# Kernel tuning notes

Hardware: AMD Instinct MI355X
Metric: run time of the kernel (lower is better)

## Reference

```python
import jax, jax.numpy as jnp
import numpy as np

TOKENS = 32768
HIDDEN = 2048
N_EXPERTS = 128
TOP_K = 8
NORM_TOPK_PROB = True


def setup_inputs() -> dict:
    key = jax.random.key(0)
    k1, k2 = jax.random.split(key)
    hidden_states = jax.random.normal(k1, (TOKENS, HIDDEN), dtype=jnp.float32)
    # router weight [num_experts, hidden_dim]; small init like a trained gate
    weight = jax.random.normal(k2, (N_EXPERTS, HIDDEN), dtype=jnp.float32) * 0.02
    return {"hidden_states": hidden_states, "weight": weight}


def reference(hidden_states, weight):
    # flatten tokens (already [T, H])
    x = hidden_states.reshape(-1, HIDDEN)
    # router logits: [T, E]
    logits = jnp.einsum("th,eh->te", x, weight)
    # softmax in float32 (matches dtype=torch.float)
    probs = jax.nn.softmax(logits.astype(jnp.float32), axis=-1)
    # top-k over experts
    top_val, top_idx = jax.lax.top_k(probs, TOP_K)  # [T, K], [T, K]
    if NORM_TOPK_PROB:
        top_val = top_val / jnp.sum(top_val, axis=-1, keepdims=True)
    top_val = top_val.astype(probs.dtype)
    # scatter renormalized weights into dense [T, E] score tensor
    rows = jnp.arange(x.shape[0])[:, None]  # [T, 1]
    scores = jnp.zeros_like(probs).at[rows, top_idx].set(top_val)
    return scores, top_idx
```

## Files before the change

### kernel.cpp

```cpp
#include <hip/hip_runtime.h>
#include <hip/hip_bf16.h>

#define NT   32768
#define NH   2048
#define NE   128
#define TOPK 8
#define BT   64
#define BK   32
#define NKT  (NH / BK)
#define BND    6.0e-4f
#define TWO_B  (2.0f * BND)

#define WS_W_OFF   64
#define WS_REC_U32 262160

typedef __attribute__((ext_vector_type(8))) short bf16x8;
typedef __attribute__((ext_vector_type(4))) float f32x4;

static __device__ __forceinline__ unsigned short f2bf(float f) {
    __hip_bfloat16 h = __float2bfloat16(f);
    return *reinterpret_cast<unsigned short*>(&h);
}

typedef __attribute__((address_space(3))) unsigned int lds_uint;
typedef const __attribute__((address_space(1))) unsigned int glb_uint;
static __device__ __forceinline__ void gld16(const void* g, void* l) {
    __builtin_amdgcn_global_load_lds((glb_uint*)g, (lds_uint*)l, 16, 0, 0);
}

__global__ __launch_bounds__(256) void prep_w_kernel(
    const float* __restrict__ W, unsigned short* __restrict__ Wt)
{
    int g = blockIdx.x * 256 + threadIdx.x;
    int t = g >> 10;
    int m = g & 1023;
    int i = m >> 6;
    int l = m & 63;
    int r = 8 * i + (l >> 3);
    int u = (l & 7) ^ (l >> 3);
    int s = u >> 2;
    int koff = (u & 3) * 8;
    const float* src = W + (size_t)r * NH + t * BK + koff;
    float4 f0 = *(const float4*)src;
    float4 f1 = *(const float4*)(src + 4);
    float f[8] = {f0.x, f0.y, f0.z, f0.w, f1.x, f1.y, f1.z, f1.w};
    bf16x8 o;
    #pragma unroll
    for (int e = 0; e < 8; ++e) {
        unsigned short h = f2bf(f[e]);
        if (s == 0) o[e] = (short)h;
        else {
            float fh = __builtin_bit_cast(float, ((unsigned int)h) << 16);
            o[e] = (short)f2bf(f[e] - fh);
        }
    }
    *(bf16x8*)(Wt + (size_t)g * 8) = o;
}

__global__ __launch_bounds__(256, 2) void router_gemm_kernel(
    const float* __restrict__ X, const unsigned short* __restrict__ Wt,
    float* __restrict__ out, unsigned int* __restrict__ ws)
{
    __shared__ __align__(16) char smem[49152];

    const int tid  = threadIdx.x;
    const int t0   = blockIdx.x * BT;
    const int lane = tid & 63;
    const int wid  = tid >> 6;
    const int wr   = wid >> 1, wc = wid & 1;
    const int l15  = lane & 15, lhi = lane >> 4;
    const int l8   = lane >> 3, l7 = lane & 7;
    const int xu   = l7 ^ l8;

    const char* Xg = (const char*)X;
    const char* Wg = (const char*)Wt;

    f32x4 acc[2][4];
    #pragma unroll
    for (int i = 0; i < 2; ++i)
        #pragma unroll
        for (int j = 0; j < 4; ++j) acc[i][j] = (f32x4){0.f, 0.f, 0.f, 0.f};

    #define STAGE(KT, B) do {                                                   \
        char* Xb_ = smem + (B) * 24576;                                         \
        char* Wb_ = Xb_ + 8192;                                                 \
        _Pragma("unroll")                                                       \
        for (int q = 0; q < 2; ++q) {                                           \
            int i_ = wid * 2 + q;                                               \
            const char* s_ = Xg + (size_t)(t0 + 8 * i_ + l8) * 8192             \
                             + (size_t)(KT) * 128 + xu * 16;                    \
            gld16(s_, Xb_ + i_ * 1024);                                         \
        }                                                                       \
        _Pragma("unroll")                                                       \
        for (int q = 0; q < 4; ++q) {                                           \
            int i_ = wid * 4 + q;                                               \
            const char* s_ = Wg + (size_t)(KT) * 16384 + i_ * 1024 + lane * 16; \
            gld16(s_, Wb_ + i_ * 1024);                                         \
        }                                                                       \
    } while (0)

    STAGE(0, 0);
    __syncthreads();

    for (int kt = 0; kt < NKT; ++kt) {
        const int cur = kt & 1;
        if (kt + 1 < NKT) STAGE(kt + 1, cur ^ 1);

        const char* Xb = smem + cur * 24576;
        const char* Wb = Xb + 8192;

        bf16x8 ah[2], al[2];
        #pragma unroll
        for (int i = 0; i < 2; ++i) {
            int ar = wr * 32 + i * 16 + l15;
            int r7 = ar & 7;
            const char* rp = Xb + ar * 128;
            float4 fa = *(const float4*)(rp + (((2 * lhi) ^ r7) * 16));
            float4 fb = *(const float4*)(rp + (((2 * lhi + 1) ^ r7) * 16));
            float f[8] = {fa.x, fa.y, fa.z, fa.w, fb.x, fb.y, fb.z, fb.w};
            #pragma unroll
            for (int e = 0; e < 8; ++e) {
                unsigned short h = f2bf(f[e]);
                ah[i][e] = (short)h;
                float fh = __builtin_bit_cast(float, ((unsigned int)h) << 16);
                al[i][e] = (short)f2bf(f[e] - fh);
            }
        }
        bf16x8 bw[4][2];
        #pragma unroll
        for (int j = 0; j < 4; ++j) {
            int br = wc * 64 + j * 16 + l15;
            int r7 = br & 7;
            const char* rp = Wb + br * 128;
            bw[j][0] = *(const bf16x8*)(rp + ((lhi ^ r7) * 16));
            bw[j][1] = *(const bf16x8*)(rp + (((4 + lhi) ^ r7) * 16));
        }
        #pragma unroll
        for (int i = 0; i < 2; ++i)
            #pragma unroll
            for (int j = 0; j < 4; ++j) {
                acc[i][j] = __builtin_amdgcn_mfma_f32_16x16x32_bf16(ah[i], bw[j][0], acc[i][j], 0, 0, 0);
                acc[i][j] = __builtin_amdgcn_mfma_f32_16x16x32_bf16(al[i], bw[j][0], acc[i][j], 0, 0, 0);
                acc[i][j] = __builtin_amdgcn_mfma_f32_16x16x32_bf16(ah[i], bw[j][1], acc[i][j], 0, 0, 0);
            }
        __syncthreads();
    }

    float* lg = (float*)smem;
    #pragma unroll
    for (int i = 0; i < 2; ++i)
        #pragma unroll
        for (int j = 0; j < 4; ++j)
            #pragma unroll
            for (int q = 0; q < 4; ++q) {
                int tr = wr * 32 + i * 16 + lhi * 4 + q;
                int ec = wc * 64 + j * 16 + l15;
                lg[tr * 129 + ec] = acc[i][j][q];
            }

    float* scoreBase = out + (size_t)t0 * NE;
    #pragma unroll
    for (int q = 0; q < 8; ++q) {
        int i = tid + q * 256;
        *(float4*)(scoreBase + (size_t)i * 4) = make_float4(0.f, 0.f, 0.f, 0.f);
    }
    __syncthreads();

    if (tid < BT) {
        const float* row = lg + tid * 129;
        float tv[13]; int ti[13];
        #pragma unroll
        for (int k = 0; k < 13; ++k) { tv[k] = -3.0e38f; ti[k] = 0; }
        for (int e = 0; e < NE; ++e) {
            float v = row[e];
            if (v > tv[12]) {
                float cv = v; int ci = e;
                #pragma unroll
                for (int s = 0; s < 13; ++s) {
                    if (cv > tv[s]) {
                        float t1 = tv[s]; int t2 = ti[s];
                        tv[s] = cv; ti[s] = ci; cv = t1; ci = t2;
                    }
                }
            }
        }
        bool flag = false;
        #pragma unroll
        for (int k = 0; k < 8; ++k) flag |= (tv[k] - tv[k + 1] < TWO_B);

        float pv[8]; float ksum = 0.f;
        #pragma unroll
        for (int k = 0; k < 8; ++k) { pv[k] = expf(tv[k] - tv[0]); ksum += pv[k]; }
        const int tg = t0 + tid;
        float* srow = out + (size_t)tg * NE;
        float* irow = out + (size_t)NT * NE + (size_t)tg * TOPK;
        #pragma unroll
        for (int k = 0; k < 8; ++k) {
            srow[ti[k]] = pv[k] / ksum;
            irow[k] = (float)ti[k];
        }

        if (flag) {
            unsigned int cnt;
            unsigned int idw[4] = {0u, 0u, 0u, 0u};
            float thr = tv[7] - TWO_B;
            if (tv[12] >= thr) {
                cnt = 0xFFu;
            } else {
                cnt = 0;
                #pragma unroll
                for (int k = 0; k < 13; ++k) {
                    if (k < 8 || tv[k] >= thr) {
                        idw[cnt >> 2] |= ((unsigned int)ti[k]) << ((cnt & 3) * 8);
                        ++cnt;
                    }
                }
            }
            unsigned int slot = atomicAdd(ws, 1u);
            unsigned int* rec = ws + WS_REC_U32 + slot * 8;
            rec[0] = (unsigned int)tg;
            rec[1] = cnt;
            rec[2] = idw[0]; rec[3] = idw[1]; rec[4] = idw[2]; rec[5] = idw[3];
        }
    }
}

__global__ __launch_bounds__(256) void finalize_kernel(
    const float* __restrict__ X, const float* __restrict__ W,
    float* __restrict__ out, const unsigned int* __restrict__ ws)
{
    __shared__ float  xs[2048];
    __shared__ double cv[128];
    __shared__ int    cid[128];
    __shared__ float  ovals[8];
    __shared__ int    oidx[8];

    const int tid = threadIdx.x;
    const int lane = tid & 63, w = tid >> 6;
    const unsigned int n = ws[0];

    for (unsigned int rI = blockIdx.x; rI < n; rI += gridDim.x) {
        const unsigned int* rec = ws + WS_REC_U32 + rI * 8;
        const int tg = (int)rec[0];
        const unsigned int cnt = rec[1];
        const unsigned char* ids = (const unsigned char*)(rec + 2);
        const int nc = (cnt == 0xFFu) ? NE : (int)cnt;

        #pragma unroll
        for (int q = 0; q < 2; ++q) {
            int i = tid + q * 256;
            *(float4*)(xs + i * 4) = *(const float4*)(X + (size_t)tg * NH + i * 4);
        }
        __syncthreads();

        for (int c = w; c < nc; c += 4) {
            int e = (cnt == 0xFFu) ? c : (int)ids[c];
            const float* wrow = W + (size_t)e * NH;
            double s = 0.0;
            #pragma unroll
            for (int m = 0; m < 8; ++m) {
                float4 wv = *(const float4*)(wrow + m * 256 + lane * 4);
                float4 xv = *(const float4*)(xs + m * 256 + lane * 4);
                s = fma((double)xv.x, (double)wv.x, s);
                s = fma((double)xv.y, (double)wv.y, s);
                s = fma((double)xv.z, (double)wv.z, s);
                s = fma((double)xv.w, (double)wv.w, s);
            }
            #pragma unroll
            for (int off = 32; off >= 1; off >>= 1) s += __shfl_xor(s, off);
            if (lane == 0) { cv[c] = s; cid[c] = e; }
        }
        __syncthreads();

        if (tid == 0) {
            double lv[8];
            #pragma unroll
            for (int k = 0; k < 8; ++k) {
                double best = -1.0e300; int bi = 1 << 30, bc = 0;
                for (int c = 0; c < nc; ++c) {
                    double v = cv[c]; int e = cid[c];
                    if (v > best || (v == best && e < bi)) { best = v; bi = e; bc = c; }
                }
                lv[k] = best; oidx[k] = bi; cv[bc] = -1.0e301;
            }
            double m = lv[0], sum = 0.0, p[8];
            #pragma unroll
            for (int k = 0; k < 8; ++k) { p[k] = exp(lv[k] - m); sum += p[k]; }
            #pragma unroll
            for (int k = 0; k < 8; ++k) ovals[k] = (float)(p[k] / sum);
        }
        __syncthreads();

        float* srow = out + (size_t)tg * NE;
        if (tid < NE) {
            float val = 0.f;
            #pragma unroll
            for (int k = 0; k < 8; ++k) if (oidx[k] == tid) val = ovals[k];
            srow[tid] = val;
        }
        if (tid < TOPK) out[(size_t)NT * NE + (size_t)tg * TOPK + tid] = (float)oidx[tid];
        __syncthreads();
    }
}

extern "C" void kernel_launch(void* const* d_in, const int* in_sizes, int n_in,
                              void* d_out, int out_size, void* d_ws, size_t ws_size,
                              hipStream_t stream) {
    const float* X = (const float*)d_in[0];
    const float* W = (const float*)d_in[1];
    float* out = (float*)d_out;
    unsigned char* wsb = (unsigned char*)d_ws;
    unsigned short* Wt = (unsigned short*)(wsb + WS_W_OFF);

    hipMemsetAsync(d_ws, 0, 64, stream);
    prep_w_kernel<<<256, 256, 0, stream>>>(W, Wt);
    router_gemm_kernel<<<NT / BT, 256, 0, stream>>>(X, Wt, out, (unsigned int*)d_ws);
    finalize_kernel<<<1024, 256, 0, stream>>>(X, W, out, (const unsigned int*)d_ws);
}
```

Measured before the change: 232.2 us.

## Use 512-thread blocks with triple-buffered LDS pipeline and fine-grained vmcnt waits

The router GEMM block grows from 256 to 512 threads, so each of the 8 waves computes a 16x64 tile instead of 32x64. The LDS double buffer becomes a rotating triple buffer that prefetches two k-tiles ahead. The full __syncthreads is replaced with s_waitcnt vmcnt(3) plus a raw barrier, so loads for the newest stage can stay in flight. The aim is more latency hiding and more waves, at the cost of more LDS per block (72KB), less register reuse per wave, and a pipeline whose correctness depends on the exact vmcnt counts.

```diff
diff --git a/kernel.cpp b/kernel.cpp
--- a/kernel.cpp
+++ b/kernel.cpp
@@ -8,6 +8,7 @@
 #define BT   64
 #define BK   32
 #define NKT  (NH / BK)
+#define BUFB 24576
 #define BND    6.0e-4f
 #define TWO_B  (2.0f * BND)
 
@@ -57,11 +58,11 @@
     *(bf16x8*)(Wt + (size_t)g * 8) = o;
 }
 
-__global__ __launch_bounds__(256, 2) void router_gemm_kernel(
+__global__ __launch_bounds__(512, 4) void router_gemm_kernel(
     const float* __restrict__ X, const unsigned short* __restrict__ Wt,
     float* __restrict__ out, unsigned int* __restrict__ ws)
 {
-    __shared__ __align__(16) char smem[49152];
+    __shared__ __align__(16) char smem[73728];
 
     const int tid  = threadIdx.x;
     const int t0   = blockIdx.x * BT;
@@ -75,44 +76,39 @@
     const char* Xg = (const char*)X;
     const char* Wg = (const char*)Wt;
 
-    f32x4 acc[2][4];
+    f32x4 acc[4];
     #pragma unroll
-    for (int i = 0; i < 2; ++i)
-        #pragma unroll
-        for (int j = 0; j < 4; ++j) acc[i][j] = (f32x4){0.f, 0.f, 0.f, 0.f};
-
-    #define STAGE(KT, B) do {                                                   \
-        char* Xb_ = smem + (B) * 24576;                                         \
-        char* Wb_ = Xb_ + 8192;                                                 \
-        _Pragma("unroll")                                                       \
-        for (int q = 0; q < 2; ++q) {                                           \
-            int i_ = wid * 2 + q;                                               \
-            const char* s_ = Xg + (size_t)(t0 + 8 * i_ + l8) * 8192             \
-                             + (size_t)(KT) * 128 + xu * 16;                    \
-            gld16(s_, Xb_ + i_ * 1024);                                         \
-        }                                                                       \
-        _Pragma("unroll")                                                       \
-        for (int q = 0; q < 4; ++q) {                                           \
-            int i_ = wid * 4 + q;                                               \
-            const char* s_ = Wg + (size_t)(KT) * 16384 + i_ * 1024 + lane * 16; \
-            gld16(s_, Wb_ + i_ * 1024);                                         \
-        }                                                                       \
-    } while (0)
-
-    STAGE(0, 0);
-    __syncthreads();
-
+    for (int j = 0; j < 4; ++j) acc[j] = (f32x4){0.f, 0.f, 0.f, 0.f};
+
+    auto stage = [&](int kt, char* base) {
+        char* Xb_ = base;
+        char* Wb_ = base + 8192;
+        const char* sx_ = Xg + (size_t)(t0 + 8 * wid + l8) * 8192
+                          + (size_t)kt * 128 + xu * 16;
+        gld16(sx_, Xb_ + wid * 1024);
+        #pragma unroll
+        for (int q = 0; q < 2; ++q) {
+            int i_ = wid * 2 + q;
+            gld16(Wg + (size_t)kt * 16384 + i_ * 1024 + lane * 16, Wb_ + i_ * 1024);
+        }
+    };
+
+    stage(0, smem);
+    stage(1, smem + BUFB);
+    asm volatile("s_waitcnt vmcnt(3)" ::: "memory");
+    __builtin_amdgcn_s_barrier();
+
+    int rd = 0, st = 2 * BUFB;
     for (int kt = 0; kt < NKT; ++kt) {
-        const int cur = kt & 1;
-        if (kt + 1 < NKT) STAGE(kt + 1, cur ^ 1);
-
-        const char* Xb = smem + cur * 24576;
+        const bool do_stage = (kt + 2 < NKT);
+        if (do_stage) stage(kt + 2, smem + st);
+
+        const char* Xb = smem + rd;
         const char* Wb = Xb + 8192;
 
-        bf16x8 ah[2], al[2];
-        #pragma unroll
-        for (int i = 0; i < 2; ++i) {
-            int ar = wr * 32 + i * 16 + l15;
+        bf16x8 ah, al;
+        {
+            int ar = wr * 16 + l15;
             int r7 = ar & 7;
             const char* rp = Xb + ar * 128;
             float4 fa = *(const float4*)(rp + (((2 * lhi) ^ r7) * 16));
@@ -121,9 +117,9 @@
             #pragma unroll
             for (int e = 0; e < 8; ++e) {
                 unsigned short h = f2bf(f[e]);
-                ah[i][e] = (short)h;
+                ah[e] = (short)h;
                 float fh = __builtin_bit_cast(float, ((unsigned int)h) << 16);
-                al[i][e] = (short)f2bf(f[e] - fh);
+                al[e] = (short)f2bf(f[e] - fh);
             }
         }
         bf16x8 bw[4][2];
@@ -136,32 +132,34 @@
             bw[j][1] = *(const bf16x8*)(rp + (((4 + lhi) ^ r7) * 16));
         }
         #pragma unroll
-        for (int i = 0; i < 2; ++i)
-            #pragma unroll
-            for (int j = 0; j < 4; ++j) {
-                acc[i][j] = __builtin_amdgcn_mfma_f32_16x16x32_bf16(ah[i], bw[j][0], acc[i][j], 0, 0, 0);
-                acc[i][j] = __builtin_amdgcn_mfma_f32_16x16x32_bf16(al[i], bw[j][0], acc[i][j], 0, 0, 0);
-                acc[i][j] = __builtin_amdgcn_mfma_f32_16x16x32_bf16(ah[i], bw[j][1], acc[i][j], 0, 0, 0);
-            }
-        __syncthreads();
+        for (int j = 0; j < 4; ++j) {
+            acc[j] = __builtin_amdgcn_mfma_f32_16x16x32_bf16(ah, bw[j][0], acc[j], 0, 0, 0);
+            acc[j] = __builtin_amdgcn_mfma_f32_16x16x32_bf16(al, bw[j][0], acc[j], 0, 0, 0);
+            acc[j] = __builtin_amdgcn_mfma_f32_16x16x32_bf16(ah, bw[j][1], acc[j], 0, 0, 0);
+        }
+
+        if (do_stage) asm volatile("s_waitcnt vmcnt(3)" ::: "memory");
+        else          asm volatile("s_waitcnt vmcnt(0)" ::: "memory");
+        __builtin_amdgcn_s_barrier();
+
+        rd = (rd == 2 * BUFB) ? 0 : rd + BUFB;
+        st = (st == 2 * BUFB) ? 0 : st + BUFB;
     }
 
     float* lg = (float*)smem;
     #pragma unroll
-    for (int i = 0; i < 2; ++i)
-        #pragma unroll
-        for (int j = 0; j < 4; ++j)
-            #pragma unroll
-            for (int q = 0; q < 4; ++q) {
-                int tr = wr * 32 + i * 16 + lhi * 4 + q;
-                int ec = wc * 64 + j * 16 + l15;
-                lg[tr * 129 + ec] = acc[i][j][q];
-            }
+    for (int j = 0; j < 4; ++j)
+        #pragma unroll
+        for (int q = 0; q < 4; ++q) {
+            int tr = wr * 16 + lhi * 4 + q;
+            int ec = wc * 64 + j * 16 + l15;
+            lg[tr * 129 + ec] = acc[j][q];
+        }
 
     float* scoreBase = out + (size_t)t0 * NE;
     #pragma unroll
-    for (int q = 0; q < 8; ++q) {
-        int i = tid + q * 256;
+    for (int q = 0; q < 4; ++q) {
+        int i = tid + q * 512;
         *(float4*)(scoreBase + (size_t)i * 4) = make_float4(0.f, 0.f, 0.f, 0.f);
     }
     __syncthreads();
@@ -314,6 +312,6 @@
 
     hipMemsetAsync(d_ws, 0, 64, stream);
     prep_w_kernel<<<256, 256, 0, stream>>>(W, Wt);
-    router_gemm_kernel<<<NT / BT, 256, 0, stream>>>(X, Wt, out, (unsigned int*)d_ws);
+    router_gemm_kernel<<<NT / BT, 512, 0, stream>>>(X, Wt, out, (unsigned int*)d_ws);
     finalize_kernel<<<1024, 256, 0, stream>>>(X, W, out, (const unsigned int*)d_ws);
 }
```

New measurement: 230.3 us. About the same (-0.8%).

## Split K across waves with direct global loads and LDS reduction of partials

Applied to the files above, without the earlier changes.

Replaces the LDS double-buffered tile GEMM (64-token blocks, K-loop over 32-wide tiles) with 32-token blocks where each of four waves handles a quarter of the hidden dimension, loading X and pre-laid-out W fragments directly from global memory into registers. Partial logits are then summed across waves through shared memory before the existing top-k stage. The weight prep layout is changed to match MFMA fragment order, and occupancy is raised to three blocks per CU. This removes the LDS staging and per-tile barriers, at the cost of uncoalesced X loads, W being re-read from L2 by twice as many blocks, and an extra reduction step.

```diff
diff --git a/kernel.cpp b/kernel.cpp
--- a/kernel.cpp
+++ b/kernel.cpp
@@ -5,9 +5,7 @@
 #define NH   2048
 #define NE   128
 #define TOPK 8
-#define BT   64
-#define BK   32
-#define NKT  (NH / BK)
+#define BT   32
 #define BND    6.0e-4f
 #define TWO_B  (2.0f * BND)
 
@@ -20,27 +18,19 @@
 static __device__ __forceinline__ unsigned short f2bf(float f) {
     __hip_bfloat16 h = __float2bfloat16(f);
     return *reinterpret_cast<unsigned short*>(&h);
-}
-
-typedef __attribute__((address_space(3))) unsigned int lds_uint;
-typedef const __attribute__((address_space(1))) unsigned int glb_uint;
-static __device__ __forceinline__ void gld16(const void* g, void* l) {
-    __builtin_amdgcn_global_load_lds((glb_uint*)g, (lds_uint*)l, 16, 0, 0);
 }
 
 __global__ __launch_bounds__(256) void prep_w_kernel(
     const float* __restrict__ W, unsigned short* __restrict__ Wt)
 {
     int g = blockIdx.x * 256 + threadIdx.x;
-    int t = g >> 10;
-    int m = g & 1023;
-    int i = m >> 6;
-    int l = m & 63;
-    int r = 8 * i + (l >> 3);
-    int u = (l & 7) ^ (l >> 3);
-    int s = u >> 2;
-    int koff = (u & 3) * 8;
-    const float* src = W + (size_t)r * NH + t * BK + koff;
+    int lane = g & 63;
+    int te   = (g >> 6) & 7;
+    int s    = (g >> 9) & 1;
+    int k32  = g >> 10;
+    int row  = te * 16 + (lane & 15);
+    int kb   = k32 * 32 + (lane >> 4) * 8;
+    const float* src = W + (size_t)row * NH + kb;
     float4 f0 = *(const float4*)src;
     float4 f1 = *(const float4*)(src + 4);
     float f[8] = {f0.x, f0.y, f0.z, f0.w, f1.x, f1.y, f1.z, f1.w};
@@ -57,66 +47,37 @@
     *(bf16x8*)(Wt + (size_t)g * 8) = o;
 }
 
-__global__ __launch_bounds__(256, 2) void router_gemm_kernel(
+__global__ __launch_bounds__(256, 3) void router_gemm_kernel(
     const float* __restrict__ X, const unsigned short* __restrict__ Wt,
     float* __restrict__ out, unsigned int* __restrict__ ws)
 {
-    __shared__ __align__(16) char smem[49152];
+    __shared__ float ps[2][BT * 132];
 
     const int tid  = threadIdx.x;
+    const int lane = tid & 63;
+    const int w    = tid >> 6;
+    const int l15  = lane & 15, lhi = lane >> 4;
     const int t0   = blockIdx.x * BT;
-    const int lane = tid & 63;
-    const int wid  = tid >> 6;
-    const int wr   = wid >> 1, wc = wid & 1;
-    const int l15  = lane & 15, lhi = lane >> 4;
-    const int l8   = lane >> 3, l7 = lane & 7;
-    const int xu   = l7 ^ l8;
-
-    const char* Xg = (const char*)X;
-    const char* Wg = (const char*)Wt;
-
-    f32x4 acc[2][4];
+
+    f32x4 acc[2][8];
     #pragma unroll
     for (int i = 0; i < 2; ++i)
         #pragma unroll
-        for (int j = 0; j < 4; ++j) acc[i][j] = (f32x4){0.f, 0.f, 0.f, 0.f};
-
-    #define STAGE(KT, B) do {                                                   \
-        char* Xb_ = smem + (B) * 24576;                                         \
-        char* Wb_ = Xb_ + 8192;                                                 \
-        _Pragma("unroll")                                                       \
-        for (int q = 0; q < 2; ++q) {                                           \
-            int i_ = wid * 2 + q;                                               \
-            const char* s_ = Xg + (size_t)(t0 + 8 * i_ + l8) * 8192             \
-                             + (size_t)(KT) * 128 + xu * 16;                    \
-            gld16(s_, Xb_ + i_ * 1024);                                         \
-        }                                                                       \
-        _Pragma("unroll")                                                       \
-        for (int q = 0; q < 4; ++q) {                                           \
-            int i_ = wid * 4 + q;                                               \
-            const char* s_ = Wg + (size_t)(KT) * 16384 + i_ * 1024 + lane * 16; \
-            gld16(s_, Wb_ + i_ * 1024);                                         \
-        }                                                                       \
-    } while (0)
-
-    STAGE(0, 0);
-    __syncthreads();
-
-    for (int kt = 0; kt < NKT; ++kt) {
-        const int cur = kt & 1;
-        if (kt + 1 < NKT) STAGE(kt + 1, cur ^ 1);
-
-        const char* Xb = smem + cur * 24576;
-        const char* Wb = Xb + 8192;
-
+        for (int te = 0; te < 8; ++te) acc[i][te] = (f32x4){0.f, 0.f, 0.f, 0.f};
+
+    const float* x0 = X + (size_t)(t0 + l15) * NH + lhi * 8;
+    const float* x1 = X + (size_t)(t0 + 16 + l15) * NH + lhi * 8;
+    const int kbase = w * 512;
+
+    #pragma unroll 2
+    for (int kk = 0; kk < 16; ++kk) {
+        const int k = kbase + kk * 32;
         bf16x8 ah[2], al[2];
         #pragma unroll
         for (int i = 0; i < 2; ++i) {
-            int ar = wr * 32 + i * 16 + l15;
-            int r7 = ar & 7;
-            const char* rp = Xb + ar * 128;
-            float4 fa = *(const float4*)(rp + (((2 * lhi) ^ r7) * 16));
-            float4 fb = *(const float4*)(rp + (((2 * lhi + 1) ^ r7) * 16));
+            const float* xp = (i ? x1 : x0) + k;
+            float4 fa = *(const float4*)xp;
+            float4 fb = *(const float4*)(xp + 4);
             float f[8] = {fa.x, fa.y, fa.z, fa.w, fb.x, fb.y, fb.z, fb.w};
             #pragma unroll
             for (int e = 0; e < 8; ++e) {
@@ -126,48 +87,62 @@
                 al[i][e] = (short)f2bf(f[e] - fh);
             }
         }
-        bf16x8 bw[4][2];
-        #pragma unroll
-        for (int j = 0; j < 4; ++j) {
-            int br = wc * 64 + j * 16 + l15;
-            int r7 = br & 7;
-            const char* rp = Wb + br * 128;
-            bw[j][0] = *(const bf16x8*)(rp + ((lhi ^ r7) * 16));
-            bw[j][1] = *(const bf16x8*)(rp + (((4 + lhi) ^ r7) * 16));
-        }
+        const unsigned short* wb = Wt + (size_t)(w * 16 + kk) * 8192;
+        #pragma unroll
+        for (int te = 0; te < 8; ++te) {
+            bf16x8 bh = *(const bf16x8*)(wb + te * 512 + lane * 8);
+            bf16x8 bl = *(const bf16x8*)(wb + 4096 + te * 512 + lane * 8);
+            acc[0][te] = __builtin_amdgcn_mfma_f32_16x16x32_bf16(ah[0], bh, acc[0][te], 0, 0, 0);
+            acc[1][te] = __builtin_amdgcn_mfma_f32_16x16x32_bf16(ah[1], bh, acc[1][te], 0, 0, 0);
+            acc[0][te] = __builtin_amdgcn_mfma_f32_16x16x32_bf16(al[0], bh, acc[0][te], 0, 0, 0);
+            acc[1][te] = __builtin_amdgcn_mfma_f32_16x16x32_bf16(al[1], bh, acc[1][te], 0, 0, 0);
+            acc[0][te] = __builtin_amdgcn_mfma_f32_16x16x32_bf16(ah[0], bl, acc[0][te], 0, 0, 0);
+            acc[1][te] = __builtin_amdgcn_mfma_f32_16x16x32_bf16(ah[1], bl, acc[1][te], 0, 0, 0);
+        }
+    }
+
+    if (w < 2) {
         #pragma unroll
         for (int i = 0; i < 2; ++i)
             #pragma unroll
-            for (int j = 0; j < 4; ++j) {
-                acc[i][j] = __builtin_amdgcn_mfma_f32_16x16x32_bf16(ah[i], bw[j][0], acc[i][j], 0, 0, 0);
-                acc[i][j] = __builtin_amdgcn_mfma_f32_16x16x32_bf16(al[i], bw[j][0], acc[i][j], 0, 0, 0);
-                acc[i][j] = __builtin_amdgcn_mfma_f32_16x16x32_bf16(ah[i], bw[j][1], acc[i][j], 0, 0, 0);
-            }
-        __syncthreads();
-    }
-
-    float* lg = (float*)smem;
-    #pragma unroll
-    for (int i = 0; i < 2; ++i)
-        #pragma unroll
-        for (int j = 0; j < 4; ++j)
-            #pragma unroll
-            for (int q = 0; q < 4; ++q) {
-                int tr = wr * 32 + i * 16 + lhi * 4 + q;
-                int ec = wc * 64 + j * 16 + l15;
-                lg[tr * 129 + ec] = acc[i][j][q];
-            }
-
+            for (int te = 0; te < 8; ++te)
+                #pragma unroll
+                for (int q = 0; q < 4; ++q)
+                    ps[w][(i * 16 + lhi * 4 + q) * 132 + te * 16 + l15] = acc[i][te][q];
+    }
+    __syncthreads();
+    if (w >= 2) {
+        #pragma unroll
+        for (int i = 0; i < 2; ++i)
+            #pragma unroll
+            for (int te = 0; te < 8; ++te)
+                #pragma unroll
+                for (int q = 0; q < 4; ++q) {
+                    int o = (i * 16 + lhi * 4 + q) * 132 + te * 16 + l15;
+                    ps[w - 2][o] += acc[i][te][q];
+                }
+    }
+    __syncthreads();
+    #pragma unroll
+    for (int q = 0; q < 4; ++q) {
+        int idx = tid + q * 256;
+        int row = idx >> 5, c4 = idx & 31;
+        int o = row * 132 + c4 * 4;
+        float4 a = *(float4*)&ps[0][o];
+        float4 b = *(float4*)&ps[1][o];
+        a.x += b.x; a.y += b.y; a.z += b.z; a.w += b.w;
+        *(float4*)&ps[0][o] = a;
+    }
     float* scoreBase = out + (size_t)t0 * NE;
     #pragma unroll
-    for (int q = 0; q < 8; ++q) {
+    for (int q = 0; q < 4; ++q) {
         int i = tid + q * 256;
         *(float4*)(scoreBase + (size_t)i * 4) = make_float4(0.f, 0.f, 0.f, 0.f);
     }
     __syncthreads();
 
     if (tid < BT) {
-        const float* row = lg + tid * 129;
+        const float* row = &ps[0][tid * 132];
         float tv[13]; int ti[13];
         #pragma unroll
         for (int k = 0; k < 13; ++k) { tv[k] = -3.0e38f; ti[k] = 0; }
```

Result: faster. 196.8 us (-15.2%).
